# Optimization experiments

Hardware: AMD Instinct MI355X
Metric: run time of the kernel (lower is better)

## Reference

```python
import jax, jax.numpy as jnp
import numpy as np
from jax import lax

N, DEG = 32768, 16

def _leaky(x):
    return jnp.where(x > 0, x, 0.2 * x)

def _gatv2(h, src, ws, bs, wd, bd, attn, bias):
    # DGL GATv2Conv: e_uv = attn . leaky_relu(fc_src(h_u) + fc_dst(h_v)); edge softmax over in-neighbors
    Hn, Dn = attn.shape
    fs = (h @ ws + bs).reshape(N, Hn, Dn)
    fd = (h @ wd + bd).reshape(N, Hn, Dn)
    e = _leaky(fs[src] + fd[:, None])                          # [N, DEG, H, D]
    alpha = jax.nn.softmax(jnp.einsum('ndhk,hk->ndh', e, attn), axis=1)
    return jnp.einsum('ndh,ndhk->nhk', alpha, fs[src]) + bias.reshape(1, Hn, Dn)

def _lstm_last(x, wih, whh, b):
    # torch LSTM gate order i,f,g,o; returns final hidden state. x: [N, DEG, F]
    n, hh = x.shape[0], whh.shape[1]
    def step(carry, xt):
        h, c = carry
        g = xt @ wih.T + h @ whh.T + b
        i, f, gg, o = jnp.split(g, 4, axis=-1)
        c = jax.nn.sigmoid(f) * c + jax.nn.sigmoid(i) * jnp.tanh(gg)
        h = jax.nn.sigmoid(o) * jnp.tanh(c)
        return (h, c), None
    init = (jnp.zeros((n, hh), x.dtype), jnp.zeros((n, hh), x.dtype))
    (h, _), _ = lax.scan(step, init, jnp.swapaxes(x, 0, 1))
    return h

def _sage(h, src, wih, whh, b, wself, wneigh, bias):
    # DGL SAGEConv(aggregator='lstm'): rst = fc_self(h) + fc_neigh(lstm(neighbor msgs))
    hn = _lstm_last(h[src], wih, whh, b)
    return h @ wself + hn @ wneigh + bias

def _forward(feat, g0, l0, g1, l1, g2, l2, s1, s2, f1_w, f1_b, f2_w, f2_b, src):
    h = feat
    h = jax.nn.elu(_gatv2(h, src, *g0).reshape(N, -1) + h @ l0[0] + l0[1])
    h = jax.nn.elu(_gatv2(h, src, *g1).reshape(N, -1) + h @ l1[0] + l1[1])
    gat = _gatv2(h, src, *g2).mean(axis=1) + h @ l2[0] + l2[1]   # [N, 32]
    x = jax.nn.relu(_sage(feat, src, *s1))
    x = jax.nn.relu(_sage(x, src, *s2))                          # [N, 32]
    z = jnp.concatenate([gat, x], axis=1)
    z = jax.nn.relu(z @ f1_w + f1_b)
    return z @ f2_w + f2_b                                       # [N, 1]

def setup_inputs() -> dict:
    ks = iter(jax.random.split(jax.random.key(0), 64))
    def nrm(shape, s=0.1):
        return (s * jax.random.normal(next(ks), shape)).astype(jnp.float32)
    d = {}
    d['feat'] = jax.random.normal(next(ks), (N, 5), jnp.float32)
    d['src'] = jax.random.randint(next(ks), (N, DEG), 0, N)
    for i, (fi, hn) in enumerate([(5, 4), (128, 4), (128, 1)]):
        fo = 32 * hn
        d[f'g{i}_ws'] = nrm((fi, fo)); d[f'g{i}_bs'] = nrm((fo,))
        d[f'g{i}_wd'] = nrm((fi, fo)); d[f'g{i}_bd'] = nrm((fo,))
        d[f'g{i}_attn'] = nrm((hn, 32)); d[f'g{i}_bias'] = nrm((fo,))
        d[f'l{i}_w'] = nrm((fi, fo)); d[f'l{i}_b'] = nrm((fo,))
    for j, fi in [(1, 5), (2, 32)]:
        d[f's{j}_wih'] = nrm((4 * fi, fi)); d[f's{j}_whh'] = nrm((4 * fi, fi))
        d[f's{j}_b'] = nrm((4 * fi,))
        d[f's{j}_wself'] = nrm((fi, 32)); d[f's{j}_wneigh'] = nrm((fi, 32))
        d[f's{j}_bias'] = nrm((32,))
    d['f1_w'] = nrm((64, 16)); d['f1_b'] = nrm((16,))
    d['f2_w'] = (0.1 + 0.01 * jax.random.normal(next(ks), (16, 1))).astype(jnp.float32)
    d['f2_b'] = nrm((1,))
    return d

def reference(feat, src, g0_ws, g0_bs, g0_wd, g0_bd, g0_attn, g0_bias, l0_w, l0_b, g1_ws, g1_bs, g1_wd, g1_bd, g1_attn, g1_bias, l1_w, l1_b, g2_ws, g2_bs, g2_wd, g2_bd, g2_attn, g2_bias, l2_w, l2_b, s1_wih, s1_whh, s1_b, s1_wself, s1_wneigh, s1_bias, s2_wih, s2_whh, s2_b, s2_wself, s2_wneigh, s2_bias, f1_w, f1_b, f2_w, f2_b):
    return _forward(feat,
                    (g0_ws, g0_bs, g0_wd, g0_bd, g0_attn, g0_bias), (l0_w, l0_b),
                    (g1_ws, g1_bs, g1_wd, g1_bd, g1_attn, g1_bias), (l1_w, l1_b),
                    (g2_ws, g2_bs, g2_wd, g2_bd, g2_attn, g2_bias), (l2_w, l2_b),
                    (s1_wih, s1_whh, s1_b, s1_wself, s1_wneigh, s1_bias),
                    (s2_wih, s2_whh, s2_b, s2_wself, s2_wneigh, s2_bias),
                    f1_w, f1_b, f2_w, f2_b, src)
```

## Files before the change

### kernel.cpp

```cpp
#include <hip/hip_runtime.h>
#include <hip/hip_bf16.h>

#define NNODES 32768
#define DEG 16

__device__ __forceinline__ float sigmoidf_(float x) { return 1.f / (1.f + __expf(-x)); }
__device__ __forceinline__ float tanhf_(float x) { return 1.f - 2.f / (__expf(2.f * x) + 1.f); }

typedef __attribute__((ext_vector_type(8))) short bf16x8;
typedef __attribute__((ext_vector_type(4))) float f32x4;

__device__ __forceinline__ unsigned short f2bf_(float x) {
  __hip_bfloat16 b = __float2bfloat16(x);
  union { __hip_bfloat16 b; unsigned short u; } cv;
  cv.b = b;
  return cv.u;
}
__device__ __forceinline__ float bf2f_(unsigned short u) {
  union { unsigned short u; __hip_bfloat16 b; } cv;
  cv.u = u;
  return __bfloat162float(cv.b);
}
__device__ __forceinline__ void pack_hilo_(const float* v, bf16x8& hi, bf16x8& lo) {
#pragma unroll
  for (int j = 0; j < 8; j++) {
    unsigned short h = f2bf_(v[j]);
    float resid = v[j] - bf2f_(h);
    hi[j] = (short)h;
    lo[j] = (short)f2bf_(resid);
  }
}

#define WP_G1    0
#define WP_G2    98304
#define WP_S2WIH 122880
#define WP_TOTAL 131072

__global__ __launch_bounds__(256) void startup_kernel(
    const float* __restrict__ feat,
    const float* __restrict__ W0, const float* __restrict__ B0,
    const float* __restrict__ W1, const float* __restrict__ B1,
    const float* __restrict__ W2, const float* __restrict__ B2,
    float* __restrict__ O0, float* __restrict__ O1, float* __restrict__ O2,
    const float* __restrict__ g1ws, const float* __restrict__ g1wd,
    const float* __restrict__ l1w, const float* __restrict__ g2ws,
    const float* __restrict__ g2wd, const float* __restrict__ l2w,
    const float* __restrict__ s2wih, short* __restrict__ Wp) {
  __shared__ float w_s[5 * 64];
  __shared__ float in_s[32 * 8];
  __shared__ float b_s[64];
  const int bid = blockIdx.x;
  const int t = threadIdx.x;
  if (bid < 6144) {
    const int bz = bid >> 11, rem = bid & 2047, by = rem >> 10, bx = rem & 1023;
    const float* W = (bz == 0) ? W0 : (bz == 1) ? W1 : W2;
    const float* bias = (bz == 0) ? B0 : (bz == 1) ? B1 : B2;
    float* out = (bz == 0) ? O0 : (bz == 1) ? O1 : O2;
    const int rowBase = bx * 32;
    const int colBase = by * 64;
    for (int idx = t; idx < 5 * 64; idx += 256) {
      int k = idx >> 6, jj = idx & 63;
      w_s[idx] = W[(size_t)k * 128 + colBase + jj];
    }
    if (t < 64) b_s[t] = bias[colBase + t];
    for (int idx = t; idx < 32 * 5; idx += 256) {
      int r = idx / 5, k = idx - r * 5;
      in_s[r * 8 + k] = feat[(size_t)(rowBase + r) * 5 + k];
    }
    __syncthreads();
    const int jj = t & 63;
    const int rslot = t >> 6;
    float acc[8];
#pragma unroll
    for (int r = 0; r < 8; r++) acc[r] = b_s[jj];
    {
      float wv0 = w_s[0 * 64 + jj], wv1 = w_s[1 * 64 + jj];
      float wv2 = w_s[2 * 64 + jj], wv3 = w_s[3 * 64 + jj];
#pragma unroll
      for (int r = 0; r < 8; r++) {
        float4 ip = *(const float4*)&in_s[(rslot * 8 + r) * 8];
        acc[r] += ip.x * wv0 + ip.y * wv1 + ip.z * wv2 + ip.w * wv3;
      }
      float wv4 = w_s[4 * 64 + jj];
#pragma unroll
      for (int r = 0; r < 8; r++) acc[r] += in_s[(rslot * 8 + r) * 8 + 4] * wv4;
    }
#pragma unroll
    for (int r = 0; r < 8; r++)
      out[(size_t)(rowBase + rslot * 8 + r) * 128 + colBase + jj] = acc[r];
  } else {
    const int mid = bid - 6144;
    const float* W;
    int FI, FO, TRANS;
    size_t base;
    if (mid == 0)      { W = g1ws;  FI = 128; FO = 128; TRANS = 0; base = WP_G1; }
    else if (mid == 1) { W = g1wd;  FI = 128; FO = 128; TRANS = 0; base = WP_G1 + 32768; }
    else if (mid == 2) { W = l1w;   FI = 128; FO = 128; TRANS = 0; base = WP_G1 + 65536; }
    else if (mid == 3) { W = g2ws;  FI = 128; FO = 32;  TRANS = 0; base = WP_G2; }
    else if (mid == 4) { W = g2wd;  FI = 128; FO = 32;  TRANS = 0; base = WP_G2 + 8192; }
    else if (mid == 5) { W = l2w;   FI = 128; FO = 32;  TRANS = 0; base = WP_G2 + 16384; }
    else               { W = s2wih; FI = 32;  FO = 128; TRANS = 1; base = WP_S2WIH; }
    const int KS = FI / 32;
    const int total = FI * FO;
    for (int p = t; p < total; p += 256) {
      int j = p & 7, lane = (p >> 3) & 63, rest = p >> 9;
      int ks = rest % KS, f = rest / KS;
      int n = lane & 15, q = lane >> 4;
      int k = 32 * ks + 8 * q + j, fo = 16 * f + n;
      float v = TRANS ? W[(size_t)fo * FI + k] : W[(size_t)k * FO + fo];
      unsigned short hi = f2bf_(v);
      float resid = v - bf2f_(hi);
      Wp[base + p] = (short)hi;
      Wp[base + total + p] = (short)f2bf_(resid);
    }
  }
}

template <int KS, int FOT, int NZ>
__global__ __launch_bounds__(256) __attribute__((amdgpu_waves_per_eu(1, 4)))
void mfma_fc_kernel(const float* __restrict__ in, const short* __restrict__ Wp,
                    const float* __restrict__ B0, const float* __restrict__ B1,
                    const float* __restrict__ B2, float* __restrict__ O0,
                    float* __restrict__ O1, float* __restrict__ O2) {
  constexpr int FI = 32 * KS;
  constexpr int FO = 16 * FOT;
  __shared__ float lds_pad[9600];
  if ((const void*)in == nullptr) lds_pad[0] = 1.f;
  const int tid = threadIdx.x;
  const int wid = tid >> 6;
  const int lane = tid & 63;
  const int q = lane >> 4, n = lane & 15;
  const int n0 = blockIdx.x * 64 + wid * 16;
  bf16x8 Ahi[KS], Alo[KS];
#pragma unroll
  for (int ks = 0; ks < KS; ks++) {
    float av[8];
    *(float4*)&av[0] = *(const float4*)&in[(size_t)(n0 + n) * FI + 32 * ks + 8 * q];
    *(float4*)&av[4] = *(const float4*)&in[(size_t)(n0 + n) * FI + 32 * ks + 8 * q + 4];
    pack_hilo_(av, Ahi[ks], Alo[ks]);
  }
#pragma unroll
  for (int z = 0; z < NZ; z++) {
    const short* wz = Wp + (size_t)z * FI * FO * 2;
    const float* bz = (z == 0) ? B0 : (z == 1) ? B1 : B2;
    float* oz = (z == 0) ? O0 : (z == 1) ? O1 : O2;
#pragma unroll
    for (int f = 0; f < FOT; f++) {
      float bv = bz[16 * f + n];
      f32x4 acc = {bv, bv, bv, bv};
#pragma unroll
      for (int ks = 0; ks < KS; ks++) {
        bf16x8 Bhi = *(const bf16x8*)&wz[((size_t)(f * KS + ks) * 64 + lane) * 8];
        bf16x8 Blo = *(const bf16x8*)&wz[(size_t)FI * FO + ((size_t)(f * KS + ks) * 64 + lane) * 8];
        acc = __builtin_amdgcn_mfma_f32_16x16x32_bf16(Ahi[ks], Bhi, acc, 0, 0, 0);
        acc = __builtin_amdgcn_mfma_f32_16x16x32_bf16(Alo[ks], Bhi, acc, 0, 0, 0);
        acc = __builtin_amdgcn_mfma_f32_16x16x32_bf16(Ahi[ks], Blo, acc, 0, 0, 0);
      }
#pragma unroll
      for (int r = 0; r < 4; r++)
        oz[(size_t)(n0 + 4 * q + r) * FO + 16 * f + n] = acc[r];
    }
  }
}

__global__ __launch_bounds__(256) void gat4_kernel(const float* __restrict__ fs,
                                                   const float* __restrict__ fd,
                                                   const float* __restrict__ lin,
                                                   const int* __restrict__ src,
                                                   const float* __restrict__ attn,
                                                   const float* __restrict__ bias,
                                                   float* __restrict__ out) {
  constexpr int F = 128;
  const int lane = threadIdx.x & 63;
  const int wave = threadIdx.x >> 6;
  const int li = lane & 15;
  const int node = blockIdx.x * 4 + wave;
  const int f0 = 2 * lane;
  const int srcv = src[(size_t)node * DEG + li];
  const float2 fdv = *(const float2*)&fd[(size_t)node * F + f0];
  const float a0 = attn[f0];
  const float a1 = attn[f0 + 1];
  float m = -1e30f, s = 0.f, acc0 = 0.f, acc1 = 0.f;
  int sd = __shfl(srcv, (lane & 48), 64);
  float2 fsv = *(const float2*)&fs[(size_t)sd * F + f0];
#pragma unroll
  for (int d = 0; d < DEG; d++) {
    float2 cur = fsv;
    if (d < DEG - 1) {
      int sn = __shfl(srcv, (lane & 48) | (d + 1), 64);
      fsv = *(const float2*)&fs[(size_t)sn * F + f0];
    }
    float e0 = cur.x + fdv.x; e0 = (e0 > 0.f) ? e0 : 0.2f * e0;
    float e1 = cur.y + fdv.y; e1 = (e1 > 0.f) ? e1 : 0.2f * e1;
    float p = e0 * a0 + e1 * a1;
    p += __shfl_xor(p, 1, 64);
    p += __shfl_xor(p, 2, 64);
    p += __shfl_xor(p, 4, 64);
    p += __shfl_xor(p, 8, 64);
    float nm = fmaxf(m, p);
    float ex = __expf(p - nm);
    float sc = __expf(m - nm);
    s = s * sc + ex;
    acc0 = acc0 * sc + ex * cur.x;
    acc1 = acc1 * sc + ex * cur.y;
    m = nm;
  }
  float inv = 1.f / s;
  float2 lv = *(const float2*)&lin[(size_t)node * F + f0];
  float o0 = acc0 * inv + lv.x + bias[f0];
  float o1 = acc1 * inv + lv.y + bias[f0 + 1];
  o0 = (o0 > 0.f) ? o0 : __expf(o0) - 1.f;
  o1 = (o1 > 0.f) ? o1 : __expf(o1) - 1.f;
  *(float2*)&out[(size_t)node * F + f0] = make_float2(o0, o1);
}

__global__ __launch_bounds__(256) void gat1_fw1_kernel(
    const float* __restrict__ fs, const float* __restrict__ fd,
    const float* __restrict__ lin, const int* __restrict__ src,
    const float* __restrict__ attn, const float* __restrict__ bias,
    float* __restrict__ out, const float* __restrict__ feat,
    const float* __restrict__ wih, const float* __restrict__ wb,
    float* __restrict__ fwout) {
  __shared__ float w_s[100];
  __shared__ float b_s[20];
  if (blockIdx.x < 2048) {
    constexpr int F = 32;
    const int lane = threadIdx.x & 63;
    const int wave = threadIdx.x >> 6;
    const int G = lane >> 4, li = lane & 15;
    const int node = blockIdx.x * 16 + wave * 4 + G;
    const int f0 = 2 * li;
    const int srcv = src[(size_t)node * DEG + li];
    const float2 fdv = *(const float2*)&fd[(size_t)node * F + f0];
    const float a0 = attn[f0];
    const float a1 = attn[f0 + 1];
    float m = -1e30f, s = 0.f, acc0 = 0.f, acc1 = 0.f;
    int sd = __shfl(srcv, (lane & 48), 64);
    float2 fsv = *(const float2*)&fs[(size_t)sd * F + f0];
#pragma unroll
    for (int d = 0; d < DEG; d++) {
      float2 cur = fsv;
      if (d < DEG - 1) {
        int sn = __shfl(srcv, (lane & 48) | (d + 1), 64);
        fsv = *(const float2*)&fs[(size_t)sn * F + f0];
      }
      float e0 = cur.x + fdv.x; e0 = (e0 > 0.f) ? e0 : 0.2f * e0;
      float e1 = cur.y + fdv.y; e1 = (e1 > 0.f) ? e1 : 0.2f * e1;
      float p = e0 * a0 + e1 * a1;
      p += __shfl_xor(p, 1, 64);
      p += __shfl_xor(p, 2, 64);
      p += __shfl_xor(p, 4, 64);
      p += __shfl_xor(p, 8, 64);
      float nm = fmaxf(m, p);
      float ex = __expf(p - nm);
      float sc = __expf(m - nm);
      s = s * sc + ex;
      acc0 = acc0 * sc + ex * cur.x;
      acc1 = acc1 * sc + ex * cur.y;
      m = nm;
    }
    float inv = 1.f / s;
    float2 lv = *(const float2*)&lin[(size_t)node * F + f0];
    float o0 = acc0 * inv + lv.x + bias[f0];
    float o1 = acc1 * inv + lv.y + bias[f0 + 1];
    *(float2*)&out[(size_t)node * F + f0] = make_float2(o0, o1);
  } else {
    if (threadIdx.x < 100) w_s[threadIdx.x] = wih[threadIdx.x];
    if (threadIdx.x < 20) b_s[threadIdx.x] = wb[threadIdx.x];
    __syncthreads();
    const int n = (blockIdx.x - 2048) * 256 + threadIdx.x;
    float f[5];
#pragma unroll
    for (int k = 0; k < 5; k++) f[k] = feat[(size_t)n * 5 + k];
#pragma unroll
    for (int j = 0; j < 20; j++) {
      float a = b_s[j];
#pragma unroll
      for (int k = 0; k < 5; k++) a += f[k] * w_s[j * 5 + k];
      fwout[(size_t)n * 20 + j] = a;
    }
  }
}

__global__ __attribute__((amdgpu_waves_per_eu(1, 4))) __launch_bounds__(256)
void lstm1s_kernel(const float* __restrict__ FW, const int* __restrict__ src,
                   const float* __restrict__ whh, const float* __restrict__ feat,
                   const float* __restrict__ wself, const float* __restrict__ wneigh,
                   const float* __restrict__ bias, float* __restrict__ x1out) {
  __shared__ float w_s[100];
  __shared__ float ws_s[160];
  __shared__ float wn_s[160];
  __shared__ float b_s[32];
  if (threadIdx.x < 100) w_s[threadIdx.x] = whh[threadIdx.x];
  if (threadIdx.x < 160) {
    ws_s[threadIdx.x] = wself[threadIdx.x];
    wn_s[threadIdx.x] = wneigh[threadIdx.x];
  }
  if (threadIdx.x < 32) b_s[threadIdx.x] = bias[threadIdx.x];
  __syncthreads();
  const int n = blockIdx.x * 256 + threadIdx.x;
  const int* sp = src + (size_t)n * DEG;
  float f[5];
#pragma unroll
  for (int k = 0; k < 5; k++) f[k] = feat[(size_t)n * 5 + k];
  float h[5] = {0, 0, 0, 0, 0}, c[5] = {0, 0, 0, 0, 0};
  int sd = sp[0];
  float4 p0 = *(const float4*)&FW[(size_t)sd * 20 + 0];
  float4 p1 = *(const float4*)&FW[(size_t)sd * 20 + 4];
  float4 p2 = *(const float4*)&FW[(size_t)sd * 20 + 8];
  float4 p3 = *(const float4*)&FW[(size_t)sd * 20 + 12];
  float4 p4 = *(const float4*)&FW[(size_t)sd * 20 + 16];
  for (int d = 0; d < DEG; d++) {
    float g[20];
    g[0] = p0.x; g[1] = p0.y; g[2] = p0.z; g[3] = p0.w;
    g[4] = p1.x; g[5] = p1.y; g[6] = p1.z; g[7] = p1.w;
    g[8] = p2.x; g[9] = p2.y; g[10] = p2.z; g[11] = p2.w;
    g[12] = p3.x; g[13] = p3.y; g[14] = p3.z; g[15] = p3.w;
    g[16] = p4.x; g[17] = p4.y; g[18] = p4.z; g[19] = p4.w;
    if (d < DEG - 1) {
      int sn = sp[d + 1];
      p0 = *(const float4*)&FW[(size_t)sn * 20 + 0];
      p1 = *(const float4*)&FW[(size_t)sn * 20 + 4];
      p2 = *(const float4*)&FW[(size_t)sn * 20 + 8];
      p3 = *(const float4*)&FW[(size_t)sn * 20 + 12];
      p4 = *(const float4*)&FW[(size_t)sn * 20 + 16];
    }
#pragma unroll
    for (int j = 0; j < 20; j++) {
#pragma unroll
      for (int k = 0; k < 5; k++) g[j] += h[k] * w_s[j * 5 + k];
    }
#pragma unroll
    for (int k = 0; k < 5; k++) {
      float iv = sigmoidf_(g[k]);
      float fv = sigmoidf_(g[5 + k]);
      float gv = tanhf_(g[10 + k]);
      float ov = sigmoidf_(g[15 + k]);
      c[k] = fv * c[k] + iv * gv;
      h[k] = ov * tanhf_(c[k]);
    }
  }
#pragma unroll
  for (int j = 0; j < 32; j++) {
    float a = b_s[j];
#pragma unroll
    for (int k = 0; k < 5; k++) a += f[k] * ws_s[k * 32 + j] + h[k] * wn_s[k * 32 + j];
    x1out[(size_t)n * 32 + j] = fmaxf(a, 0.f);
  }
}

__global__ __launch_bounds__(256) __attribute__((amdgpu_waves_per_eu(1, 2)))
void lstm2_mfma_kernel(const float* __restrict__ XW, const int* __restrict__ src,
                       const float* __restrict__ whh, float* __restrict__ hn_out) {
  __shared__ float h_lds_all[4 * 16 * 36];
  __shared__ int src_lds_all[4 * 256];
  __shared__ float lds_pad[15000];
  if ((const void*)XW == nullptr) lds_pad[0] = 1.f;
  const int tid = threadIdx.x;
  const int wid = tid >> 6;
  const int lane = tid & 63;
  const int q = lane >> 4;
  const int n = lane & 15;
  const int n0 = (blockIdx.x * 4 + wid) * 16;
  float* h_lds = &h_lds_all[wid * 16 * 36];
  int* src_lds = &src_lds_all[wid * 256];

  {
    int4 sv = *(const int4*)&src[(size_t)(n0 + (lane >> 2)) * DEG + 4 * (lane & 3)];
    src_lds[(4 * (lane & 3) + 0) * 16 + (lane >> 2)] = sv.x;
    src_lds[(4 * (lane & 3) + 1) * 16 + (lane >> 2)] = sv.y;
    src_lds[(4 * (lane & 3) + 2) * 16 + (lane >> 2)] = sv.z;
    src_lds[(4 * (lane & 3) + 3) * 16 + (lane >> 2)] = sv.w;
  }

  bf16x8 Whi[8], Wlo[8];
#pragma unroll
  for (int gt = 0; gt < 8; gt++) {
    float wv[8];
    *(float4*)&wv[0] = *(const float4*)&whh[(size_t)(16 * gt + n) * 32 + 8 * q];
    *(float4*)&wv[4] = *(const float4*)&whh[(size_t)(16 * gt + n) * 32 + 8 * q + 4];
    pack_hilo_(wv, Whi[gt], Wlo[gt]);
  }

  bf16x8 Bhi, Blo;
#pragma unroll
  for (int j = 0; j < 8; j++) { Bhi[j] = 0; Blo[j] = 0; }
  float cst[8];
#pragma unroll
  for (int i = 0; i < 8; i++) cst[i] = 0.f;

  float4 tc[8], tn[8];
  {
    int s0 = src_lds[0 * 16 + n];
    const float* gb = XW + (size_t)s0 * 128;
#pragma unroll
    for (int i = 0; i < 8; i++) tc[i] = *(const float4*)&gb[16 * i + 4 * q];
  }

  float hv[8];
#pragma unroll
  for (int d = 0; d < DEG; d++) {
    f32x4 D[4][2];
#pragma unroll
    for (int p = 0; p < 4; p++) {
#pragma unroll
      for (int hh = 0; hh < 2; hh++) {
        int gt = p * 2 + hh;
        f32x4 acc = {0.f, 0.f, 0.f, 0.f};
        acc = __builtin_amdgcn_mfma_f32_16x16x32_bf16(Whi[gt], Bhi, acc, 0, 0, 0);
        acc = __builtin_amdgcn_mfma_f32_16x16x32_bf16(Wlo[gt], Bhi, acc, 0, 0, 0);
        acc = __builtin_amdgcn_mfma_f32_16x16x32_bf16(Whi[gt], Blo, acc, 0, 0, 0);
        D[p][hh] = acc;
      }
    }
    if (d < DEG - 1) {
      int s = src_lds[(d + 1) * 16 + n];
      const float* gb = XW + (size_t)s * 128;
#pragma unroll
      for (int i = 0; i < 8; i++) tn[i] = *(const float4*)&gb[16 * i + 4 * q];
    }
#pragma unroll
    for (int hh = 0; hh < 2; hh++) {
      float4 xi = tc[0 + hh];
      float4 xf = tc[2 + hh];
      float4 xg = tc[4 + hh];
      float4 xo = tc[6 + hh];
#pragma unroll
      for (int r = 0; r < 4; r++) {
        float xiv = (r == 0) ? xi.x : (r == 1) ? xi.y : (r == 2) ? xi.z : xi.w;
        float xfv = (r == 0) ? xf.x : (r == 1) ? xf.y : (r == 2) ? xf.z : xf.w;
        float xgv = (r == 0) ? xg.x : (r == 1) ? xg.y : (r == 2) ? xg.z : xg.w;
        float xov = (r == 0) ? xo.x : (r == 1) ? xo.y : (r == 2) ? xo.z : xo.w;
        int ci = hh * 4 + r;
        float iv = sigmoidf_(D[0][hh][r] + xiv);
        float fv = sigmoidf_(D[1][hh][r] + xfv);
        float gv = tanhf_(D[2][hh][r] + xgv);
        float ov = sigmoidf_(D[3][hh][r] + xov);
        cst[ci] = fv * cst[ci] + iv * gv;
        hv[ci] = ov * tanhf_(cst[ci]);
      }
    }
    if (d < DEG - 1) {
      *(float4*)&h_lds[n * 36 + 0 + 4 * q] = make_float4(hv[0], hv[1], hv[2], hv[3]);
      *(float4*)&h_lds[n * 36 + 16 + 4 * q] = make_float4(hv[4], hv[5], hv[6], hv[7]);
      float hb[8];
      *(float4*)&hb[0] = *(const float4*)&h_lds[n * 36 + 8 * q];
      *(float4*)&hb[4] = *(const float4*)&h_lds[n * 36 + 8 * q + 4];
      pack_hilo_(hb, Bhi, Blo);
#pragma unroll
      for (int i = 0; i < 8; i++) tc[i] = tn[i];
    }
  }
  *(float4*)&hn_out[(size_t)(n0 + n) * 32 + 0 + 4 * q] = make_float4(hv[0], hv[1], hv[2], hv[3]);
  *(float4*)&hn_out[(size_t)(n0 + n) * 32 + 16 + 4 * q] = make_float4(hv[4], hv[5], hv[6], hv[7]);
}

template <int FI>
__global__ __launch_bounds__(256) void sage_out_kernel(const float* __restrict__ in,
                                                       const float* __restrict__ hn,
                                                       const float* __restrict__ wself,
                                                       const float* __restrict__ wneigh,
                                                       const float* __restrict__ bias,
                                                       float* __restrict__ out) {
  __shared__ float ws_s[FI * 32];
  __shared__ float wn_s[FI * 32];
  __shared__ float b_s[32];
  for (int idx = threadIdx.x; idx < FI * 32; idx += 256) {
    ws_s[idx] = wself[idx];
    wn_s[idx] = wneigh[idx];
  }
  if (threadIdx.x < 32) b_s[threadIdx.x] = bias[threadIdx.x];
  __syncthreads();
  const int n = blockIdx.x * 8 + (threadIdx.x >> 5);
  const int j = threadIdx.x & 31;
  float a = b_s[j];
#pragma unroll
  for (int k = 0; k < FI; k++) a += in[(size_t)n * FI + k] * ws_s[k * 32 + j];
#pragma unroll
  for (int k = 0; k < FI; k++) a += hn[(size_t)n * FI + k] * wn_s[k * 32 + j];
  out[(size_t)n * 32 + j] = fmaxf(a, 0.f);
}

__global__ __attribute__((amdgpu_waves_per_eu(4, 4))) __launch_bounds__(256)
void final_kernel(const float* __restrict__ gat,
                  const float* __restrict__ x2,
                  const float* __restrict__ f1w,
                  const float* __restrict__ f1b,
                  const float* __restrict__ f2w,
                  const float* __restrict__ f2b,
                  float* __restrict__ out) {
  __shared__ float w1_s[64 * 16];
  __shared__ float b1_s[16];
  __shared__ float w2_s[16];
  for (int idx = threadIdx.x; idx < 1024; idx += 256) w1_s[idx] = f1w[idx];
  if (threadIdx.x < 16) {
    b1_s[threadIdx.x] = f1b[threadIdx.x];
    w2_s[threadIdx.x] = f2w[threadIdx.x];
  }
  __syncthreads();
  const int n = blockIdx.x * 256 + threadIdx.x;
  float z[64];
#pragma unroll
  for (int k = 0; k < 32; k += 4) {
    float4 a = *(const float4*)&gat[(size_t)n * 32 + k];
    z[k] = a.x; z[k + 1] = a.y; z[k + 2] = a.z; z[k + 3] = a.w;
    float4 b = *(const float4*)&x2[(size_t)n * 32 + k];
    z[32 + k] = b.x; z[32 + k + 1] = b.y; z[32 + k + 2] = b.z; z[32 + k + 3] = b.w;
  }
  float o = f2b[0];
#pragma unroll
  for (int j = 0; j < 16; j++) {
    float a = b1_s[j];
#pragma unroll
    for (int k = 0; k < 64; k++) a += z[k] * w1_s[k * 16 + j];
    o += fmaxf(a, 0.f) * w2_s[j];
  }
  out[n] = o;
}

extern "C" void kernel_launch(void* const* d_in, const int* in_sizes, int n_in,
                              void* d_out, int out_size, void* d_ws, size_t ws_size,
                              hipStream_t stream) {
  const int N = NNODES;
  const float* feat = (const float*)d_in[0];
  const int* src = (const int*)d_in[1];
  const float* g0_ws = (const float*)d_in[2];
  const float* g0_bs = (const float*)d_in[3];
  const float* g0_wd = (const float*)d_in[4];
  const float* g0_bd = (const float*)d_in[5];
  const float* g0_attn = (const float*)d_in[6];
  const float* g0_bias = (const float*)d_in[7];
  const float* l0_w = (const float*)d_in[8];
  const float* l0_b = (const float*)d_in[9];
  const float* g1_ws = (const float*)d_in[10];
  const float* g1_bs = (const float*)d_in[11];
  const float* g1_wd = (const float*)d_in[12];
  const float* g1_bd = (const float*)d_in[13];
  const float* g1_attn = (const float*)d_in[14];
  const float* g1_bias = (const float*)d_in[15];
  const float* l1_w = (const float*)d_in[16];
  const float* l1_b = (const float*)d_in[17];
  const float* g2_ws = (const float*)d_in[18];
  const float* g2_bs = (const float*)d_in[19];
  const float* g2_wd = (const float*)d_in[20];
  const float* g2_bd = (const float*)d_in[21];
  const float* g2_attn = (const float*)d_in[22];
  const float* g2_bias = (const float*)d_in[23];
  const float* l2_w = (const float*)d_in[24];
  const float* l2_b = (const float*)d_in[25];
  const float* s1_wih = (const float*)d_in[26];
  const float* s1_whh = (const float*)d_in[27];
  const float* s1_b = (const float*)d_in[28];
  const float* s1_wself = (const float*)d_in[29];
  const float* s1_wneigh = (const float*)d_in[30];
  const float* s1_bias = (const float*)d_in[31];
  const float* s2_wih = (const float*)d_in[32];
  const float* s2_whh = (const float*)d_in[33];
  const float* s2_b = (const float*)d_in[34];
  const float* s2_wself = (const float*)d_in[35];
  const float* s2_wneigh = (const float*)d_in[36];
  const float* s2_bias = (const float*)d_in[37];
  const float* f1_w = (const float*)d_in[38];
  const float* f1_b = (const float*)d_in[39];
  const float* f2_w = (const float*)d_in[40];
  const float* f2_b = (const float*)d_in[41];

  float* A = (float*)d_ws;
  float* B = A + (size_t)N * 128;
  float* C = B + (size_t)N * 128;
  float* D = C + (size_t)N * 128;
  float* E = D + (size_t)N * 128;
  short* Wp = (short*)(A + (size_t)5 * N * 128);

  startup_kernel<<<6151, 256, 0, stream>>>(
      feat, g0_ws, g0_bs, g0_wd, g0_bd, l0_w, l0_b, A, B, C,
      g1_ws, g1_wd, l1_w, g2_ws, g2_wd, l2_w, s2_wih, Wp);
  gat4_kernel<<<N / 4, 256, 0, stream>>>(A, B, C, src, g0_attn, g0_bias, D);
  mfma_fc_kernel<4, 8, 3><<<N / 64, 256, 0, stream>>>(
      D, Wp + WP_G1, g1_bs, g1_bd, l1_b, A, B, C);
  gat4_kernel<<<N / 4, 256, 0, stream>>>(A, B, C, src, g1_attn, g1_bias, E);
  mfma_fc_kernel<4, 2, 3><<<N / 64, 256, 0, stream>>>(
      E, Wp + WP_G2, g2_bs, g2_bd, l2_b, A, B, C);
  gat1_fw1_kernel<<<2048 + 128, 256, 0, stream>>>(
      A, B, C, src, g2_attn, g2_bias, D, feat, s1_wih, s1_b, E);
  lstm1s_kernel<<<N / 256, 256, 0, stream>>>(E, src, s1_whh, feat, s1_wself,
                                             s1_wneigh, s1_bias, C);
  mfma_fc_kernel<1, 8, 1><<<N / 64, 256, 0, stream>>>(
      C, Wp + WP_S2WIH, s2_b, nullptr, nullptr, A, nullptr, nullptr);
  lstm2_mfma_kernel<<<N / 64, 256, 0, stream>>>(A, src, s2_whh, E);
  sage_out_kernel<32><<<N / 8, 256, 0, stream>>>(C, E, s2_wself, s2_wneigh,
                                                 s2_bias, B);
  final_kernel<<<N / 256, 256, 0, stream>>>(D, B, f1_w, f1_b, f2_w, f2_b, (float*)d_out);
}
```

Baseline: 424.7 us.

## Interleave independent SAGE/LSTM branch work into GAT kernels via horizontal fusion

The independent SAGE-LSTM branch is co-scheduled with the GAT layers. Block indices are split inside merged kernels so that GAT and LSTM1, the FC layer and the XW projection, GAT and LSTM2, and the FC layer and the SAGE output run in the same launches, which cuts the kernel count from eleven to seven. The point is to fill idle CUs during the long serial LSTM recurrences and to save launch gaps. The price is extra workspace buffers; a fallback keeps the old path when the workspace is too small, and the merged kernels may have uneven block costs and more LDS per block.

```diff
diff --git a/kernel.cpp b/kernel.cpp
--- a/kernel.cpp
+++ b/kernel.cpp
@@ -35,6 +35,373 @@
 #define WP_G2    98304
 #define WP_S2WIH 122880
 #define WP_TOTAL 131072
+
+
+__device__ __forceinline__ void gat4_body(int vbid, const float* __restrict__ fs,
+                                          const float* __restrict__ fd,
+                                          const float* __restrict__ lin,
+                                          const int* __restrict__ src,
+                                          const float* __restrict__ attn,
+                                          const float* __restrict__ bias,
+                                          float* __restrict__ out) {
+  constexpr int F = 128;
+  const int lane = threadIdx.x & 63;
+  const int wave = threadIdx.x >> 6;
+  const int li = lane & 15;
+  const int node = vbid * 4 + wave;
+  const int f0 = 2 * lane;
+  const int srcv = src[(size_t)node * DEG + li];
+  const float2 fdv = *(const float2*)&fd[(size_t)node * F + f0];
+  const float a0 = attn[f0];
+  const float a1 = attn[f0 + 1];
+  float m = -1e30f, s = 0.f, acc0 = 0.f, acc1 = 0.f;
+  int sd = __shfl(srcv, (lane & 48), 64);
+  float2 fsv = *(const float2*)&fs[(size_t)sd * F + f0];
+#pragma unroll
+  for (int d = 0; d < DEG; d++) {
+    float2 cur = fsv;
+    if (d < DEG - 1) {
+      int sn = __shfl(srcv, (lane & 48) | (d + 1), 64);
+      fsv = *(const float2*)&fs[(size_t)sn * F + f0];
+    }
+    float e0 = cur.x + fdv.x; e0 = (e0 > 0.f) ? e0 : 0.2f * e0;
+    float e1 = cur.y + fdv.y; e1 = (e1 > 0.f) ? e1 : 0.2f * e1;
+    float p = e0 * a0 + e1 * a1;
+    p += __shfl_xor(p, 1, 64);
+    p += __shfl_xor(p, 2, 64);
+    p += __shfl_xor(p, 4, 64);
+    p += __shfl_xor(p, 8, 64);
+    float nm = fmaxf(m, p);
+    float ex = __expf(p - nm);
+    float sc = __expf(m - nm);
+    s = s * sc + ex;
+    acc0 = acc0 * sc + ex * cur.x;
+    acc1 = acc1 * sc + ex * cur.y;
+    m = nm;
+  }
+  float inv = 1.f / s;
+  float2 lv = *(const float2*)&lin[(size_t)node * F + f0];
+  float o0 = acc0 * inv + lv.x + bias[f0];
+  float o1 = acc1 * inv + lv.y + bias[f0 + 1];
+  o0 = (o0 > 0.f) ? o0 : __expf(o0) - 1.f;
+  o1 = (o1 > 0.f) ? o1 : __expf(o1) - 1.f;
+  *(float2*)&out[(size_t)node * F + f0] = make_float2(o0, o1);
+}
+
+__device__ __forceinline__ void gat1_body(int vbid, const float* __restrict__ fs,
+                                          const float* __restrict__ fd,
+                                          const float* __restrict__ lin,
+                                          const int* __restrict__ src,
+                                          const float* __restrict__ attn,
+                                          const float* __restrict__ bias,
+                                          float* __restrict__ out) {
+  constexpr int F = 32;
+  const int lane = threadIdx.x & 63;
+  const int wave = threadIdx.x >> 6;
+  const int G = lane >> 4, li = lane & 15;
+  const int node = vbid * 16 + wave * 4 + G;
+  const int f0 = 2 * li;
+  const int srcv = src[(size_t)node * DEG + li];
+  const float2 fdv = *(const float2*)&fd[(size_t)node * F + f0];
+  const float a0 = attn[f0];
+  const float a1 = attn[f0 + 1];
+  float m = -1e30f, s = 0.f, acc0 = 0.f, acc1 = 0.f;
+  int sd = __shfl(srcv, (lane & 48), 64);
+  float2 fsv = *(const float2*)&fs[(size_t)sd * F + f0];
+#pragma unroll
+  for (int d = 0; d < DEG; d++) {
+    float2 cur = fsv;
+    if (d < DEG - 1) {
+      int sn = __shfl(srcv, (lane & 48) | (d + 1), 64);
+      fsv = *(const float2*)&fs[(size_t)sn * F + f0];
+    }
+    float e0 = cur.x + fdv.x; e0 = (e0 > 0.f) ? e0 : 0.2f * e0;
+    float e1 = cur.y + fdv.y; e1 = (e1 > 0.f) ? e1 : 0.2f * e1;
+    float p = e0 * a0 + e1 * a1;
+    p += __shfl_xor(p, 1, 64);
+    p += __shfl_xor(p, 2, 64);
+    p += __shfl_xor(p, 4, 64);
+    p += __shfl_xor(p, 8, 64);
+    float nm = fmaxf(m, p);
+    float ex = __expf(p - nm);
+    float sc = __expf(m - nm);
+    s = s * sc + ex;
+    acc0 = acc0 * sc + ex * cur.x;
+    acc1 = acc1 * sc + ex * cur.y;
+    m = nm;
+  }
+  float inv = 1.f / s;
+  float2 lv = *(const float2*)&lin[(size_t)node * F + f0];
+  float o0 = acc0 * inv + lv.x + bias[f0];
+  float o1 = acc1 * inv + lv.y + bias[f0 + 1];
+  *(float2*)&out[(size_t)node * F + f0] = make_float2(o0, o1);
+}
+
+template <int KS, int FOT, int NZ>
+__device__ __forceinline__ void mfma_fc_body(int vbid, const float* __restrict__ in,
+                                             const short* __restrict__ Wp,
+                                             const float* __restrict__ B0,
+                                             const float* __restrict__ B1,
+                                             const float* __restrict__ B2,
+                                             float* __restrict__ O0,
+                                             float* __restrict__ O1,
+                                             float* __restrict__ O2) {
+  constexpr int FI = 32 * KS;
+  constexpr int FO = 16 * FOT;
+  const int tid = threadIdx.x;
+  const int wid = tid >> 6;
+  const int lane = tid & 63;
+  const int q = lane >> 4, n = lane & 15;
+  const int n0 = vbid * 64 + wid * 16;
+  bf16x8 Ahi[KS], Alo[KS];
+#pragma unroll
+  for (int ks = 0; ks < KS; ks++) {
+    float av[8];
+    *(float4*)&av[0] = *(const float4*)&in[(size_t)(n0 + n) * FI + 32 * ks + 8 * q];
+    *(float4*)&av[4] = *(const float4*)&in[(size_t)(n0 + n) * FI + 32 * ks + 8 * q + 4];
+    pack_hilo_(av, Ahi[ks], Alo[ks]);
+  }
+#pragma unroll
+  for (int z = 0; z < NZ; z++) {
+    const short* wz = Wp + (size_t)z * FI * FO * 2;
+    const float* bz = (z == 0) ? B0 : (z == 1) ? B1 : B2;
+    float* oz = (z == 0) ? O0 : (z == 1) ? O1 : O2;
+#pragma unroll
+    for (int f = 0; f < FOT; f++) {
+      float bv = bz[16 * f + n];
+      f32x4 acc = {bv, bv, bv, bv};
+#pragma unroll
+      for (int ks = 0; ks < KS; ks++) {
+        bf16x8 Bhi = *(const bf16x8*)&wz[((size_t)(f * KS + ks) * 64 + lane) * 8];
+        bf16x8 Blo = *(const bf16x8*)&wz[(size_t)FI * FO + ((size_t)(f * KS + ks) * 64 + lane) * 8];
+        acc = __builtin_amdgcn_mfma_f32_16x16x32_bf16(Ahi[ks], Bhi, acc, 0, 0, 0);
+        acc = __builtin_amdgcn_mfma_f32_16x16x32_bf16(Alo[ks], Bhi, acc, 0, 0, 0);
+        acc = __builtin_amdgcn_mfma_f32_16x16x32_bf16(Ahi[ks], Blo, acc, 0, 0, 0);
+      }
+#pragma unroll
+      for (int r = 0; r < 4; r++)
+        oz[(size_t)(n0 + 4 * q + r) * FO + 16 * f + n] = acc[r];
+    }
+  }
+}
+
+__device__ __forceinline__ void fw1_body(int vbid, const float* __restrict__ feat,
+                                         const float* __restrict__ wih,
+                                         const float* __restrict__ wb,
+                                         float* __restrict__ fwout,
+                                         float* w_s, float* b_s) {
+  if (threadIdx.x < 100) w_s[threadIdx.x] = wih[threadIdx.x];
+  if (threadIdx.x < 20) b_s[threadIdx.x] = wb[threadIdx.x];
+  __syncthreads();
+  const int n = vbid * 256 + threadIdx.x;
+  float f[5];
+#pragma unroll
+  for (int k = 0; k < 5; k++) f[k] = feat[(size_t)n * 5 + k];
+#pragma unroll
+  for (int j = 0; j < 20; j++) {
+    float a = b_s[j];
+#pragma unroll
+    for (int k = 0; k < 5; k++) a += f[k] * w_s[j * 5 + k];
+    fwout[(size_t)n * 20 + j] = a;
+  }
+}
+
+__device__ __forceinline__ void lstm1s_body(int vbid, const float* __restrict__ FW,
+                                            const int* __restrict__ src,
+                                            const float* __restrict__ whh,
+                                            const float* __restrict__ feat,
+                                            const float* __restrict__ wself,
+                                            const float* __restrict__ wneigh,
+                                            const float* __restrict__ bias,
+                                            float* __restrict__ x1out,
+                                            float* w_s, float* ws_s, float* wn_s,
+                                            float* b_s) {
+  if (threadIdx.x < 100) w_s[threadIdx.x] = whh[threadIdx.x];
+  if (threadIdx.x < 160) {
+    ws_s[threadIdx.x] = wself[threadIdx.x];
+    wn_s[threadIdx.x] = wneigh[threadIdx.x];
+  }
+  if (threadIdx.x < 32) b_s[threadIdx.x] = bias[threadIdx.x];
+  __syncthreads();
+  const int n = vbid * 256 + threadIdx.x;
+  const int* sp = src + (size_t)n * DEG;
+  float f[5];
+#pragma unroll
+  for (int k = 0; k < 5; k++) f[k] = feat[(size_t)n * 5 + k];
+  float h[5] = {0, 0, 0, 0, 0}, c[5] = {0, 0, 0, 0, 0};
+  int sd = sp[0];
+  float4 p0 = *(const float4*)&FW[(size_t)sd * 20 + 0];
+  float4 p1 = *(const float4*)&FW[(size_t)sd * 20 + 4];
+  float4 p2 = *(const float4*)&FW[(size_t)sd * 20 + 8];
+  float4 p3 = *(const float4*)&FW[(size_t)sd * 20 + 12];
+  float4 p4 = *(const float4*)&FW[(size_t)sd * 20 + 16];
+  for (int d = 0; d < DEG; d++) {
+    float g[20];
+    g[0] = p0.x; g[1] = p0.y; g[2] = p0.z; g[3] = p0.w;
+    g[4] = p1.x; g[5] = p1.y; g[6] = p1.z; g[7] = p1.w;
+    g[8] = p2.x; g[9] = p2.y; g[10] = p2.z; g[11] = p2.w;
+    g[12] = p3.x; g[13] = p3.y; g[14] = p3.z; g[15] = p3.w;
+    g[16] = p4.x; g[17] = p4.y; g[18] = p4.z; g[19] = p4.w;
+    if (d < DEG - 1) {
+      int sn = sp[d + 1];
+      p0 = *(const float4*)&FW[(size_t)sn * 20 + 0];
+      p1 = *(const float4*)&FW[(size_t)sn * 20 + 4];
+      p2 = *(const float4*)&FW[(size_t)sn * 20 + 8];
+      p3 = *(const float4*)&FW[(size_t)sn * 20 + 12];
+      p4 = *(const float4*)&FW[(size_t)sn * 20 + 16];
+    }
+#pragma unroll
+    for (int j = 0; j < 20; j++) {
+#pragma unroll
+      for (int k = 0; k < 5; k++) g[j] += h[k] * w_s[j * 5 + k];
+    }
+#pragma unroll
+    for (int k = 0; k < 5; k++) {
+      float iv = sigmoidf_(g[k]);
+      float fv = sigmoidf_(g[5 + k]);
+      float gv = tanhf_(g[10 + k]);
+      float ov = sigmoidf_(g[15 + k]);
+      c[k] = fv * c[k] + iv * gv;
+      h[k] = ov * tanhf_(c[k]);
+    }
+  }
+#pragma unroll
+  for (int j = 0; j < 32; j++) {
+    float a = b_s[j];
+#pragma unroll
+    for (int k = 0; k < 5; k++) a += f[k] * ws_s[k * 32 + j] + h[k] * wn_s[k * 32 + j];
+    x1out[(size_t)n * 32 + j] = fmaxf(a, 0.f);
+  }
+}
+
+__device__ __forceinline__ void lstm2_body(int vbid, const float* __restrict__ XW,
+                                           const int* __restrict__ src,
+                                           const float* __restrict__ whh,
+                                           float* __restrict__ hn_out,
+                                           float* h_lds_all, int* src_lds_all) {
+  const int tid = threadIdx.x;
+  const int wid = tid >> 6;
+  const int lane = tid & 63;
+  const int q = lane >> 4;
+  const int n = lane & 15;
+  const int n0 = (vbid * 4 + wid) * 16;
+  float* h_lds = &h_lds_all[wid * 16 * 36];
+  int* src_lds = &src_lds_all[wid * 256];
+
+  {
+    int4 sv = *(const int4*)&src[(size_t)(n0 + (lane >> 2)) * DEG + 4 * (lane & 3)];
+    src_lds[(4 * (lane & 3) + 0) * 16 + (lane >> 2)] = sv.x;
+    src_lds[(4 * (lane & 3) + 1) * 16 + (lane >> 2)] = sv.y;
+    src_lds[(4 * (lane & 3) + 2) * 16 + (lane >> 2)] = sv.z;
+    src_lds[(4 * (lane & 3) + 3) * 16 + (lane >> 2)] = sv.w;
+  }
+
+  bf16x8 Whi[8], Wlo[8];
+#pragma unroll
+  for (int gt = 0; gt < 8; gt++) {
+    float wv[8];
+    *(float4*)&wv[0] = *(const float4*)&whh[(size_t)(16 * gt + n) * 32 + 8 * q];
+    *(float4*)&wv[4] = *(const float4*)&whh[(size_t)(16 * gt + n) * 32 + 8 * q + 4];
+    pack_hilo_(wv, Whi[gt], Wlo[gt]);
+  }
+
+  bf16x8 Bhi, Blo;
+#pragma unroll
+  for (int j = 0; j < 8; j++) { Bhi[j] = 0; Blo[j] = 0; }
+  float cst[8];
+#pragma unroll
+  for (int i = 0; i < 8; i++) cst[i] = 0.f;
+
+  float4 tc[8], tn[8];
+  {
+    int s0 = src_lds[0 * 16 + n];
+    const float* gb = XW + (size_t)s0 * 128;
+#pragma unroll
+    for (int i = 0; i < 8; i++) tc[i] = *(const float4*)&gb[16 * i + 4 * q];
+  }
+
+  float hv[8];
+#pragma unroll
+  for (int d = 0; d < DEG; d++) {
+    f32x4 D[4][2];
+#pragma unroll
+    for (int p = 0; p < 4; p++) {
+#pragma unroll
+      for (int hh = 0; hh < 2; hh++) {
+        int gt = p * 2 + hh;
+        f32x4 acc = {0.f, 0.f, 0.f, 0.f};
+        acc = __builtin_amdgcn_mfma_f32_16x16x32_bf16(Whi[gt], Bhi, acc, 0, 0, 0);
+        acc = __builtin_amdgcn_mfma_f32_16x16x32_bf16(Wlo[gt], Bhi, acc, 0, 0, 0);
+        acc = __builtin_amdgcn_mfma_f32_16x16x32_bf16(Whi[gt], Blo, acc, 0, 0, 0);
+        D[p][hh] = acc;
+      }
+    }
+    if (d < DEG - 1) {
+      int s = src_lds[(d + 1) * 16 + n];
+      const float* gb = XW + (size_t)s * 128;
+#pragma unroll
+      for (int i = 0; i < 8; i++) tn[i] = *(const float4*)&gb[16 * i + 4 * q];
+    }
+#pragma unroll
+    for (int hh = 0; hh < 2; hh++) {
+      float4 xi = tc[0 + hh];
+      float4 xf = tc[2 + hh];
+      float4 xg = tc[4 + hh];
+      float4 xo = tc[6 + hh];
+#pragma unroll
+      for (int r = 0; r < 4; r++) {
+        float xiv = (r == 0) ? xi.x : (r == 1) ? xi.y : (r == 2) ? xi.z : xi.w;
+        float xfv = (r == 0) ? xf.x : (r == 1) ? xf.y : (r == 2) ? xf.z : xf.w;
+        float xgv = (r == 0) ? xg.x : (r == 1) ? xg.y : (r == 2) ? xg.z : xg.w;
+        float xov = (r == 0) ? xo.x : (r == 1) ? xo.y : (r == 2) ? xo.z : xo.w;
+        int ci = hh * 4 + r;
+        float iv = sigmoidf_(D[0][hh][r] + xiv);
+        float fv = sigmoidf_(D[1][hh][r] + xfv);
+        float gv = tanhf_(D[2][hh][r] + xgv);
+        float ov = sigmoidf_(D[3][hh][r] + xov);
+        cst[ci] = fv * cst[ci] + iv * gv;
+        hv[ci] = ov * tanhf_(cst[ci]);
+      }
+    }
+    if (d < DEG - 1) {
+      *(float4*)&h_lds[n * 36 + 0 + 4 * q] = make_float4(hv[0], hv[1], hv[2], hv[3]);
+      *(float4*)&h_lds[n * 36 + 16 + 4 * q] = make_float4(hv[4], hv[5], hv[6], hv[7]);
+      float hb[8];
+      *(float4*)&hb[0] = *(const float4*)&h_lds[n * 36 + 8 * q];
+      *(float4*)&hb[4] = *(const float4*)&h_lds[n * 36 + 8 * q + 4];
+      pack_hilo_(hb, Bhi, Blo);
+#pragma unroll
+      for (int i = 0; i < 8; i++) tc[i] = tn[i];
+    }
+  }
+  *(float4*)&hn_out[(size_t)(n0 + n) * 32 + 0 + 4 * q] = make_float4(hv[0], hv[1], hv[2], hv[3]);
+  *(float4*)&hn_out[(size_t)(n0 + n) * 32 + 16 + 4 * q] = make_float4(hv[4], hv[5], hv[6], hv[7]);
+}
+
+__device__ __forceinline__ void sage_body(int vbid, const float* __restrict__ in,
+                                          const float* __restrict__ hn,
+                                          const float* __restrict__ wself,
+                                          const float* __restrict__ wneigh,
+                                          const float* __restrict__ bias,
+                                          float* __restrict__ out,
+                                          float* ws_s, float* wn_s, float* b_s) {
+  constexpr int FI = 32;
+  for (int idx = threadIdx.x; idx < FI * 32; idx += 256) {
+    ws_s[idx] = wself[idx];
+    wn_s[idx] = wneigh[idx];
+  }
+  if (threadIdx.x < 32) b_s[threadIdx.x] = bias[threadIdx.x];
+  __syncthreads();
+  const int n = vbid * 8 + (threadIdx.x >> 5);
+  const int j = threadIdx.x & 31;
+  float a = b_s[j];
+#pragma unroll
+  for (int k = 0; k < FI; k++) a += in[(size_t)n * FI + k] * ws_s[k * 32 + j];
+#pragma unroll
+  for (int k = 0; k < FI; k++) a += hn[(size_t)n * FI + k] * wn_s[k * 32 + j];
+  out[(size_t)n * 32 + j] = fmaxf(a, 0.f);
+}
+
 
 __global__ __launch_bounds__(256) void startup_kernel(
     const float* __restrict__ feat,
@@ -45,7 +412,9 @@
     const float* __restrict__ g1ws, const float* __restrict__ g1wd,
     const float* __restrict__ l1w, const float* __restrict__ g2ws,
     const float* __restrict__ g2wd, const float* __restrict__ l2w,
-    const float* __restrict__ s2wih, short* __restrict__ Wp) {
+    const float* __restrict__ s2wih, short* __restrict__ Wp,
+    const float* __restrict__ s1wih, const float* __restrict__ s1b,
+    float* __restrict__ fwout) {
   __shared__ float w_s[5 * 64];
   __shared__ float in_s[32 * 8];
   __shared__ float b_s[64];
@@ -88,7 +457,7 @@
 #pragma unroll
     for (int r = 0; r < 8; r++)
       out[(size_t)(rowBase + rslot * 8 + r) * 128 + colBase + jj] = acc[r];
-  } else {
+  } else if (bid < 6151) {
     const int mid = bid - 6144;
     const float* W;
     int FI, FO, TRANS;
@@ -113,53 +482,8 @@
       Wp[base + p] = (short)hi;
       Wp[base + total + p] = (short)f2bf_(resid);
     }
-  }
-}
-
-template <int KS, int FOT, int NZ>
-__global__ __launch_bounds__(256) __attribute__((amdgpu_waves_per_eu(1, 4)))
-void mfma_fc_kernel(const float* __restrict__ in, const short* __restrict__ Wp,
-                    const float* __restrict__ B0, const float* __restrict__ B1,
-                    const float* __restrict__ B2, float* __restrict__ O0,
-                    float* __restrict__ O1, float* __restrict__ O2) {
-  constexpr int FI = 32 * KS;
-  constexpr int FO = 16 * FOT;
-  __shared__ float lds_pad[9600];
-  if ((const void*)in == nullptr) lds_pad[0] = 1.f;
-  const int tid = threadIdx.x;
-  const int wid = tid >> 6;
-  const int lane = tid & 63;
-  const int q = lane >> 4, n = lane & 15;
-  const int n0 = blockIdx.x * 64 + wid * 16;
-  bf16x8 Ahi[KS], Alo[KS];
-#pragma unroll
-  for (int ks = 0; ks < KS; ks++) {
-    float av[8];
-    *(float4*)&av[0] = *(const float4*)&in[(size_t)(n0 + n) * FI + 32 * ks + 8 * q];
-    *(float4*)&av[4] = *(const float4*)&in[(size_t)(n0 + n) * FI + 32 * ks + 8 * q + 4];
-    pack_hilo_(av, Ahi[ks], Alo[ks]);
-  }
-#pragma unroll
-  for (int z = 0; z < NZ; z++) {
-    const short* wz = Wp + (size_t)z * FI * FO * 2;
-    const float* bz = (z == 0) ? B0 : (z == 1) ? B1 : B2;
-    float* oz = (z == 0) ? O0 : (z == 1) ? O1 : O2;
-#pragma unroll
-    for (int f = 0; f < FOT; f++) {
-      float bv = bz[16 * f + n];
-      f32x4 acc = {bv, bv, bv, bv};
-#pragma unroll
-      for (int ks = 0; ks < KS; ks++) {
-        bf16x8 Bhi = *(const bf16x8*)&wz[((size_t)(f * KS + ks) * 64 + lane) * 8];
-        bf16x8 Blo = *(const bf16x8*)&wz[(size_t)FI * FO + ((size_t)(f * KS + ks) * 64 + lane) * 8];
-        acc = __builtin_amdgcn_mfma_f32_16x16x32_bf16(Ahi[ks], Bhi, acc, 0, 0, 0);
-        acc = __builtin_amdgcn_mfma_f32_16x16x32_bf16(Alo[ks], Bhi, acc, 0, 0, 0);
-        acc = __builtin_amdgcn_mfma_f32_16x16x32_bf16(Ahi[ks], Blo, acc, 0, 0, 0);
-      }
-#pragma unroll
-      for (int r = 0; r < 4; r++)
-        oz[(size_t)(n0 + 4 * q + r) * FO + 16 * f + n] = acc[r];
-    }
+  } else {
+    fw1_body(bid - 6151, feat, s1wih, s1b, fwout, w_s, b_s);
   }
 }
 
@@ -170,48 +494,18 @@
                                                    const float* __restrict__ attn,
                                                    const float* __restrict__ bias,
                                                    float* __restrict__ out) {
-  constexpr int F = 128;
-  const int lane = threadIdx.x & 63;
-  const int wave = threadIdx.x >> 6;
-  const int li = lane & 15;
-  const int node = blockIdx.x * 4 + wave;
-  const int f0 = 2 * lane;
-  const int srcv = src[(size_t)node * DEG + li];
-  const float2 fdv = *(const float2*)&fd[(size_t)node * F + f0];
-  const float a0 = attn[f0];
-  const float a1 = attn[f0 + 1];
-  float m = -1e30f, s = 0.f, acc0 = 0.f, acc1 = 0.f;
-  int sd = __shfl(srcv, (lane & 48), 64);
-  float2 fsv = *(const float2*)&fs[(size_t)sd * F + f0];
-#pragma unroll
-  for (int d = 0; d < DEG; d++) {
-    float2 cur = fsv;
-    if (d < DEG - 1) {
-      int sn = __shfl(srcv, (lane & 48) | (d + 1), 64);
-      fsv = *(const float2*)&fs[(size_t)sn * F + f0];
-    }
-    float e0 = cur.x + fdv.x; e0 = (e0 > 0.f) ? e0 : 0.2f * e0;
-    float e1 = cur.y + fdv.y; e1 = (e1 > 0.f) ? e1 : 0.2f * e1;
-    float p = e0 * a0 + e1 * a1;
-    p += __shfl_xor(p, 1, 64);
-    p += __shfl_xor(p, 2, 64);
-    p += __shfl_xor(p, 4, 64);
-    p += __shfl_xor(p, 8, 64);
-    float nm = fmaxf(m, p);
-    float ex = __expf(p - nm);
-    float sc = __expf(m - nm);
-    s = s * sc + ex;
-    acc0 = acc0 * sc + ex * cur.x;
-    acc1 = acc1 * sc + ex * cur.y;
-    m = nm;
-  }
-  float inv = 1.f / s;
-  float2 lv = *(const float2*)&lin[(size_t)node * F + f0];
-  float o0 = acc0 * inv + lv.x + bias[f0];
-  float o1 = acc1 * inv + lv.y + bias[f0 + 1];
-  o0 = (o0 > 0.f) ? o0 : __expf(o0) - 1.f;
-  o1 = (o1 > 0.f) ? o1 : __expf(o1) - 1.f;
-  *(float2*)&out[(size_t)node * F + f0] = make_float2(o0, o1);
+  gat4_body(blockIdx.x, fs, fd, lin, src, attn, bias, out);
+}
+
+template <int KS, int FOT, int NZ>
+__global__ __launch_bounds__(256) __attribute__((amdgpu_waves_per_eu(1, 4)))
+void mfma_fc_kernel(const float* __restrict__ in, const short* __restrict__ Wp,
+                    const float* __restrict__ B0, const float* __restrict__ B1,
+                    const float* __restrict__ B2, float* __restrict__ O0,
+                    float* __restrict__ O1, float* __restrict__ O2) {
+  __shared__ float lds_pad[9600];
+  if ((const void*)in == nullptr) lds_pad[0] = 1.f;
+  mfma_fc_body<KS, FOT, NZ>(blockIdx.x, in, Wp, B0, B1, B2, O0, O1, O2);
 }
 
 __global__ __launch_bounds__(256) void gat1_fw1_kernel(
@@ -224,62 +518,18 @@
   __shared__ float w_s[100];
   __shared__ float b_s[20];
   if (blockIdx.x < 2048) {
-    constexpr int F = 32;
-    const int lane = threadIdx.x & 63;
-    const int wave = threadIdx.x >> 6;
-    const int G = lane >> 4, li = lane & 15;
-    const int node = blockIdx.x * 16 + wave * 4 + G;
-    const int f0 = 2 * li;
-    const int srcv = src[(size_t)node * DEG + li];
-    const float2 fdv = *(const float2*)&fd[(size_t)node * F + f0];
-    const float a0 = attn[f0];
-    const float a1 = attn[f0 + 1];
-    float m = -1e30f, s = 0.f, acc0 = 0.f, acc1 = 0.f;
-    int sd = __shfl(srcv, (lane & 48), 64);
-    float2 fsv = *(const float2*)&fs[(size_t)sd * F + f0];
-#pragma unroll
-    for (int d = 0; d < DEG; d++) {
-      float2 cur = fsv;
-      if (d < DEG - 1) {
-        int sn = __shfl(srcv, (lane & 48) | (d + 1), 64);
-        fsv = *(const float2*)&fs[(size_t)sn * F + f0];
-      }
-      float e0 = cur.x + fdv.x; e0 = (e0 > 0.f) ? e0 : 0.2f * e0;
-      float e1 = cur.y + fdv.y; e1 = (e1 > 0.f) ? e1 : 0.2f * e1;
-      float p = e0 * a0 + e1 * a1;
-      p += __shfl_xor(p, 1, 64);
-      p += __shfl_xor(p, 2, 64);
-      p += __shfl_xor(p, 4, 64);
-      p += __shfl_xor(p, 8, 64);
-      float nm = fmaxf(m, p);
-      float ex = __expf(p - nm);
-      float sc = __expf(m - nm);
-      s = s * sc + ex;
-      acc0 = acc0 * sc + ex * cur.x;
-      acc1 = acc1 * sc + ex * cur.y;
-      m = nm;
-    }
-    float inv = 1.f / s;
-    float2 lv = *(const float2*)&lin[(size_t)node * F + f0];
-    float o0 = acc0 * inv + lv.x + bias[f0];
-    float o1 = acc1 * inv + lv.y + bias[f0 + 1];
-    *(float2*)&out[(size_t)node * F + f0] = make_float2(o0, o1);
+    gat1_body(blockIdx.x, fs, fd, lin, src, attn, bias, out);
   } else {
-    if (threadIdx.x < 100) w_s[threadIdx.x] = wih[threadIdx.x];
-    if (threadIdx.x < 20) b_s[threadIdx.x] = wb[threadIdx.x];
-    __syncthreads();
-    const int n = (blockIdx.x - 2048) * 256 + threadIdx.x;
-    float f[5];
-#pragma unroll
-    for (int k = 0; k < 5; k++) f[k] = feat[(size_t)n * 5 + k];
-#pragma unroll
-    for (int j = 0; j < 20; j++) {
-      float a = b_s[j];
-#pragma unroll
-      for (int k = 0; k < 5; k++) a += f[k] * w_s[j * 5 + k];
-      fwout[(size_t)n * 20 + j] = a;
-    }
-  }
+    fw1_body(blockIdx.x - 2048, feat, wih, wb, fwout, w_s, b_s);
+  }
+}
+
+__global__ __launch_bounds__(256) void gat1_kernel(
+    const float* __restrict__ fs, const float* __restrict__ fd,
+    const float* __restrict__ lin, const int* __restrict__ src,
+    const float* __restrict__ attn, const float* __restrict__ bias,
+    float* __restrict__ out) {
+  gat1_body(blockIdx.x, fs, fd, lin, src, attn, bias, out);
 }
 
 __global__ __attribute__((amdgpu_waves_per_eu(1, 4))) __launch_bounds__(256)
@@ -291,62 +541,8 @@
   __shared__ float ws_s[160];
   __shared__ float wn_s[160];
   __shared__ float b_s[32];
-  if (threadIdx.x < 100) w_s[threadIdx.x] = whh[threadIdx.x];
-  if (threadIdx.x < 160) {
-    ws_s[threadIdx.x] = wself[threadIdx.x];
-    wn_s[threadIdx.x] = wneigh[threadIdx.x];
-  }
-  if (threadIdx.x < 32) b_s[threadIdx.x] = bias[threadIdx.x];
-  __syncthreads();
-  const int n = blockIdx.x * 256 + threadIdx.x;
-  const int* sp = src + (size_t)n * DEG;
-  float f[5];
-#pragma unroll
-  for (int k = 0; k < 5; k++) f[k] = feat[(size_t)n * 5 + k];
-  float h[5] = {0, 0, 0, 0, 0}, c[5] = {0, 0, 0, 0, 0};
-  int sd = sp[0];
-  float4 p0 = *(const float4*)&FW[(size_t)sd * 20 + 0];
-  float4 p1 = *(const float4*)&FW[(size_t)sd * 20 + 4];
-  float4 p2 = *(const float4*)&FW[(size_t)sd * 20 + 8];
-  float4 p3 = *(const float4*)&FW[(size_t)sd * 20 + 12];
-  float4 p4 = *(const float4*)&FW[(size_t)sd * 20 + 16];
-  for (int d = 0; d < DEG; d++) {
-    float g[20];
-    g[0] = p0.x; g[1] = p0.y; g[2] = p0.z; g[3] = p0.w;
-    g[4] = p1.x; g[5] = p1.y; g[6] = p1.z; g[7] = p1.w;
-    g[8] = p2.x; g[9] = p2.y; g[10] = p2.z; g[11] = p2.w;
-    g[12] = p3.x; g[13] = p3.y; g[14] = p3.z; g[15] = p3.w;
-    g[16] = p4.x; g[17] = p4.y; g[18] = p4.z; g[19] = p4.w;
-    if (d < DEG - 1) {
-      int sn = sp[d + 1];
-      p0 = *(const float4*)&FW[(size_t)sn * 20 + 0];
-      p1 = *(const float4*)&FW[(size_t)sn * 20 + 4];
-      p2 = *(const float4*)&FW[(size_t)sn * 20 + 8];
-      p3 = *(const float4*)&FW[(size_t)sn * 20 + 12];
-      p4 = *(const float4*)&FW[(size_t)sn * 20 + 16];
-    }
-#pragma unroll
-    for (int j = 0; j < 20; j++) {
-#pragma unroll
-      for (int k = 0; k < 5; k++) g[j] += h[k] * w_s[j * 5 + k];
-    }
-#pragma unroll
-    for (int k = 0; k < 5; k++) {
-      float iv = sigmoidf_(g[k]);
-      float fv = sigmoidf_(g[5 + k]);
-      float gv = tanhf_(g[10 + k]);
-      float ov = sigmoidf_(g[15 + k]);
-      c[k] = fv * c[k] + iv * gv;
-      h[k] = ov * tanhf_(c[k]);
-    }
-  }
-#pragma unroll
-  for (int j = 0; j < 32; j++) {
-    float a = b_s[j];
-#pragma unroll
-    for (int k = 0; k < 5; k++) a += f[k] * ws_s[k * 32 + j] + h[k] * wn_s[k * 32 + j];
-    x1out[(size_t)n * 32 + j] = fmaxf(a, 0.f);
-  }
+  lstm1s_body(blockIdx.x, FW, src, whh, feat, wself, wneigh, bias, x1out,
+              w_s, ws_s, wn_s, b_s);
 }
 
 __global__ __launch_bounds__(256) __attribute__((amdgpu_waves_per_eu(1, 2)))
@@ -356,129 +552,102 @@
   __shared__ int src_lds_all[4 * 256];
   __shared__ float lds_pad[15000];
   if ((const void*)XW == nullptr) lds_pad[0] = 1.f;
-  const int tid = threadIdx.x;
-  const int wid = tid >> 6;
-  const int lane = tid & 63;
-  const int q = lane >> 4;
-  const int n = lane & 15;
-  const int n0 = (blockIdx.x * 4 + wid) * 16;
-  float* h_lds = &h_lds_all[wid * 16 * 36];
-  int* src_lds = &src_lds_all[wid * 256];
-
-  {
-    int4 sv = *(const int4*)&src[(size_t)(n0 + (lane >> 2)) * DEG + 4 * (lane & 3)];
-    src_lds[(4 * (lane & 3) + 0) * 16 + (lane >> 2)] = sv.x;
-    src_lds[(4 * (lane & 3) + 1) * 16 + (lane >> 2)] = sv.y;
-    src_lds[(4 * (lane & 3) + 2) * 16 + (lane >> 2)] = sv.z;
-    src_lds[(4 * (lane & 3) + 3) * 16 + (lane >> 2)] = sv.w;
-  }
-
-  bf16x8 Whi[8], Wlo[8];
-#pragma unroll
-  for (int gt = 0; gt < 8; gt++) {
-    float wv[8];
-    *(float4*)&wv[0] = *(const float4*)&whh[(size_t)(16 * gt + n) * 32 + 8 * q];
-    *(float4*)&wv[4] = *(const float4*)&whh[(size_t)(16 * gt + n) * 32 + 8 * q + 4];
-    pack_hilo_(wv, Whi[gt], Wlo[gt]);
-  }
-
-  bf16x8 Bhi, Blo;
-#pragma unroll
-  for (int j = 0; j < 8; j++) { Bhi[j] = 0; Blo[j] = 0; }
-  float cst[8];
-#pragma unroll
-  for (int i = 0; i < 8; i++) cst[i] = 0.f;
-
-  float4 tc[8], tn[8];
-  {
-    int s0 = src_lds[0 * 16 + n];
-    const float* gb = XW + (size_t)s0 * 128;
-#pragma unroll
-    for (int i = 0; i < 8; i++) tc[i] = *(const float4*)&gb[16 * i + 4 * q];
-  }
-
-  float hv[8];
-#pragma unroll
-  for (int d = 0; d < DEG; d++) {
-    f32x4 D[4][2];
-#pragma unroll
-    for (int p = 0; p < 4; p++) {
-#pragma unroll
-      for (int hh = 0; hh < 2; hh++) {
-        int gt = p * 2 + hh;
-        f32x4 acc = {0.f, 0.f, 0.f, 0.f};
-        acc = __builtin_amdgcn_mfma_f32_16x16x32_bf16(Whi[gt], Bhi, acc, 0, 0, 0);
-        acc = __builtin_amdgcn_mfma_f32_16x16x32_bf16(Wlo[gt], Bhi, acc, 0, 0, 0);
-        acc = __builtin_amdgcn_mfma_f32_16x16x32_bf16(Whi[gt], Blo, acc, 0, 0, 0);
-        D[p][hh] = acc;
-      }
-    }
-    if (d < DEG - 1) {
-      int s = src_lds[(d + 1) * 16 + n];
-      const float* gb = XW + (size_t)s * 128;
-#pragma unroll
-      for (int i = 0; i < 8; i++) tn[i] = *(const float4*)&gb[16 * i + 4 * q];
-    }
-#pragma unroll
-    for (int hh = 0; hh < 2; hh++) {
-      float4 xi = tc[0 + hh];
-      float4 xf = tc[2 + hh];
-      float4 xg = tc[4 + hh];
-      float4 xo = tc[6 + hh];
-#pragma unroll
-      for (int r = 0; r < 4; r++) {
-        float xiv = (r == 0) ? xi.x : (r == 1) ? xi.y : (r == 2) ? xi.z : xi.w;
-        float xfv = (r == 0) ? xf.x : (r == 1) ? xf.y : (r == 2) ? xf.z : xf.w;
-        float xgv = (r == 0) ? xg.x : (r == 1) ? xg.y : (r == 2) ? xg.z : xg.w;
-        float xov = (r == 0) ? xo.x : (r == 1) ? xo.y : (r == 2) ? xo.z : xo.w;
-        int ci = hh * 4 + r;
-        float iv = sigmoidf_(D[0][hh][r] + xiv);
-        float fv = sigmoidf_(D[1][hh][r] + xfv);
-        float gv = tanhf_(D[2][hh][r] + xgv);
-        float ov = sigmoidf_(D[3][hh][r] + xov);
-        cst[ci] = fv * cst[ci] + iv * gv;
-        hv[ci] = ov * tanhf_(cst[ci]);
-      }
-    }
-    if (d < DEG - 1) {
-      *(float4*)&h_lds[n * 36 + 0 + 4 * q] = make_float4(hv[0], hv[1], hv[2], hv[3]);
-      *(float4*)&h_lds[n * 36 + 16 + 4 * q] = make_float4(hv[4], hv[5], hv[6], hv[7]);
-      float hb[8];
-      *(float4*)&hb[0] = *(const float4*)&h_lds[n * 36 + 8 * q];
-      *(float4*)&hb[4] = *(const float4*)&h_lds[n * 36 + 8 * q + 4];
-      pack_hilo_(hb, Bhi, Blo);
-#pragma unroll
-      for (int i = 0; i < 8; i++) tc[i] = tn[i];
-    }
-  }
-  *(float4*)&hn_out[(size_t)(n0 + n) * 32 + 0 + 4 * q] = make_float4(hv[0], hv[1], hv[2], hv[3]);
-  *(float4*)&hn_out[(size_t)(n0 + n) * 32 + 16 + 4 * q] = make_float4(hv[4], hv[5], hv[6], hv[7]);
-}
-
-template <int FI>
+  lstm2_body(blockIdx.x, XW, src, whh, hn_out, h_lds_all, src_lds_all);
+}
+
 __global__ __launch_bounds__(256) void sage_out_kernel(const float* __restrict__ in,
                                                        const float* __restrict__ hn,
                                                        const float* __restrict__ wself,
                                                        const float* __restrict__ wneigh,
                                                        const float* __restrict__ bias,
                                                        float* __restrict__ out) {
-  __shared__ float ws_s[FI * 32];
-  __shared__ float wn_s[FI * 32];
+  __shared__ float ws_s[32 * 32];
+  __shared__ float wn_s[32 * 32];
   __shared__ float b_s[32];
-  for (int idx = threadIdx.x; idx < FI * 32; idx += 256) {
-    ws_s[idx] = wself[idx];
-    wn_s[idx] = wneigh[idx];
-  }
-  if (threadIdx.x < 32) b_s[threadIdx.x] = bias[threadIdx.x];
-  __syncthreads();
-  const int n = blockIdx.x * 8 + (threadIdx.x >> 5);
-  const int j = threadIdx.x & 31;
-  float a = b_s[j];
-#pragma unroll
-  for (int k = 0; k < FI; k++) a += in[(size_t)n * FI + k] * ws_s[k * 32 + j];
-#pragma unroll
-  for (int k = 0; k < FI; k++) a += hn[(size_t)n * FI + k] * wn_s[k * 32 + j];
-  out[(size_t)n * 32 + j] = fmaxf(a, 0.f);
+  sage_body(blockIdx.x, in, hn, wself, wneigh, bias, out, ws_s, wn_s, b_s);
+}
+
+
+__global__ __launch_bounds__(256) void gat4_lstm1s_kernel(
+    const float* __restrict__ fs, const float* __restrict__ fd,
+    const float* __restrict__ lin, const int* __restrict__ src,
+    const float* __restrict__ attn, const float* __restrict__ bias,
+    float* __restrict__ out,
+    const float* __restrict__ FW, const float* __restrict__ whh,
+    const float* __restrict__ feat, const float* __restrict__ wself,
+    const float* __restrict__ wneigh, const float* __restrict__ sbias,
+    float* __restrict__ x1out) {
+  __shared__ float w_s[100];
+  __shared__ float ws_s[160];
+  __shared__ float wn_s[160];
+  __shared__ float b_s[32];
+  const int bid = blockIdx.x;
+  const int r = bid % 65, q = bid / 65;
+  if (r < 64) {
+    gat4_body(q * 64 + r, fs, fd, lin, src, attn, bias, out);
+  } else {
+    lstm1s_body(q, FW, src, whh, feat, wself, wneigh, sbias, x1out,
+                w_s, ws_s, wn_s, b_s);
+  }
+}
+
+__global__ __launch_bounds__(256) void mfma_g1_xw_kernel(
+    const float* __restrict__ in, const short* __restrict__ Wp,
+    const float* __restrict__ B0, const float* __restrict__ B1,
+    const float* __restrict__ B2, float* __restrict__ O0,
+    float* __restrict__ O1, float* __restrict__ O2,
+    const float* __restrict__ x1, const short* __restrict__ WpX,
+    const float* __restrict__ s2b, float* __restrict__ XW) {
+  __shared__ float lds_pad[9600];
+  if ((const void*)in == nullptr) lds_pad[0] = 1.f;
+  const int bid = blockIdx.x;
+  if ((bid & 1) == 0) {
+    mfma_fc_body<4, 8, 3>(bid >> 1, in, Wp, B0, B1, B2, O0, O1, O2);
+  } else {
+    mfma_fc_body<1, 8, 1>(bid >> 1, x1, WpX, s2b, nullptr, nullptr,
+                          XW, nullptr, nullptr);
+  }
+}
+
+__global__ __launch_bounds__(256) void gat4_lstm2_kernel(
+    const float* __restrict__ fs, const float* __restrict__ fd,
+    const float* __restrict__ lin, const int* __restrict__ src,
+    const float* __restrict__ attn, const float* __restrict__ bias,
+    float* __restrict__ out,
+    const float* __restrict__ XW, const float* __restrict__ whh,
+    float* __restrict__ hn_out) {
+  __shared__ float h_lds_all[4 * 16 * 36];
+  __shared__ int src_lds_all[4 * 256];
+  const int bid = blockIdx.x;
+  const int r = bid % 17, q = bid / 17;
+  if (r < 16) {
+    gat4_body(q * 16 + r, fs, fd, lin, src, attn, bias, out);
+  } else {
+    lstm2_body(q, XW, src, whh, hn_out, h_lds_all, src_lds_all);
+  }
+}
+
+__global__ __launch_bounds__(256) void mfma_g2_sage_kernel(
+    const float* __restrict__ in, const short* __restrict__ Wp,
+    const float* __restrict__ B0, const float* __restrict__ B1,
+    const float* __restrict__ B2, float* __restrict__ O0,
+    float* __restrict__ O1, float* __restrict__ O2,
+    const float* __restrict__ x1, const float* __restrict__ hn,
+    const float* __restrict__ wself, const float* __restrict__ wneigh,
+    const float* __restrict__ sbias, float* __restrict__ x2out) {
+  __shared__ float lds_pad[9600];
+  __shared__ float ws_s[32 * 32];
+  __shared__ float wn_s[32 * 32];
+  __shared__ float b_s[32];
+  if ((const void*)in == nullptr) lds_pad[0] = 1.f;
+  const int bid = blockIdx.x;
+  const int r = bid % 9, q = bid / 9;
+  if (r == 0) {
+    mfma_fc_body<4, 2, 3>(q, in, Wp, B0, B1, B2, O0, O1, O2);
+  } else {
+    sage_body(q * 8 + (r - 1), x1, hn, wself, wneigh, sbias, x2out,
+              ws_s, wn_s, b_s);
+  }
 }
 
 __global__ __attribute__((amdgpu_waves_per_eu(4, 4))) __launch_bounds__(256)
@@ -571,24 +740,52 @@
   float* D = C + (size_t)N * 128;
   float* E = D + (size_t)N * 128;
   short* Wp = (short*)(A + (size_t)5 * N * 128);
-
-  startup_kernel<<<6151, 256, 0, stream>>>(
-      feat, g0_ws, g0_bs, g0_wd, g0_bd, l0_w, l0_b, A, B, C,
-      g1_ws, g1_wd, l1_w, g2_ws, g2_wd, l2_w, s2_wih, Wp);
-  gat4_kernel<<<N / 4, 256, 0, stream>>>(A, B, C, src, g0_attn, g0_bias, D);
-  mfma_fc_kernel<4, 8, 3><<<N / 64, 256, 0, stream>>>(
-      D, Wp + WP_G1, g1_bs, g1_bd, l1_b, A, B, C);
-  gat4_kernel<<<N / 4, 256, 0, stream>>>(A, B, C, src, g1_attn, g1_bias, E);
-  mfma_fc_kernel<4, 2, 3><<<N / 64, 256, 0, stream>>>(
-      E, Wp + WP_G2, g2_bs, g2_bd, l2_b, A, B, C);
-  gat1_fw1_kernel<<<2048 + 128, 256, 0, stream>>>(
-      A, B, C, src, g2_attn, g2_bias, D, feat, s1_wih, s1_b, E);
-  lstm1s_kernel<<<N / 256, 256, 0, stream>>>(E, src, s1_whh, feat, s1_wself,
-                                             s1_wneigh, s1_bias, C);
-  mfma_fc_kernel<1, 8, 1><<<N / 64, 256, 0, stream>>>(
-      C, Wp + WP_S2WIH, s2_b, nullptr, nullptr, A, nullptr, nullptr);
-  lstm2_mfma_kernel<<<N / 64, 256, 0, stream>>>(A, src, s2_whh, E);
-  sage_out_kernel<32><<<N / 8, 256, 0, stream>>>(C, E, s2_wself, s2_wneigh,
-                                                 s2_bias, B);
-  final_kernel<<<N / 256, 256, 0, stream>>>(D, B, f1_w, f1_b, f2_w, f2_b, (float*)d_out);
-}
+  float* X1 = (float*)(Wp + WP_TOTAL);
+  float* XW = X1 + (size_t)N * 32;
+  float* HN2 = XW + (size_t)N * 128;
+  float* X2 = HN2 + (size_t)N * 32;
+  const size_t need = (size_t)((char*)(X2 + (size_t)N * 32) - (char*)d_ws);
+  const bool big = ws_size >= need;
+
+  if (big) {
+    startup_kernel<<<6151 + 128, 256, 0, stream>>>(
+        feat, g0_ws, g0_bs, g0_wd, g0_bd, l0_w, l0_b, A, B, C,
+        g1_ws, g1_wd, l1_w, g2_ws, g2_wd, l2_w, s2_wih, Wp, s1_wih, s1_b, E);
+    gat4_lstm1s_kernel<<<8320, 256, 0, stream>>>(
+        A, B, C, src, g0_attn, g0_bias, D,
+        E, s1_whh, feat, s1_wself, s1_wneigh, s1_bias, X1);
+    mfma_g1_xw_kernel<<<1024, 256, 0, stream>>>(
+        D, Wp + WP_G1, g1_bs, g1_bd, l1_b, A, B, C,
+        X1, Wp + WP_S2WIH, s2_b, XW);
+    gat4_lstm2_kernel<<<8704, 256, 0, stream>>>(
+        A, B, C, src, g1_attn, g1_bias, E,
+        XW, s2_whh, HN2);
+    mfma_g2_sage_kernel<<<4608, 256, 0, stream>>>(
+        E, Wp + WP_G2, g2_bs, g2_bd, l2_b, A, B, C,
+        X1, HN2, s2_wself, s2_wneigh, s2_bias, X2);
+    gat1_kernel<<<2048, 256, 0, stream>>>(A, B, C, src, g2_attn, g2_bias, D);
+    final_kernel<<<N / 256, 256, 0, stream>>>(D, X2, f1_w, f1_b, f2_w, f2_b,
+                                              (float*)d_out);
+  } else {
+    startup_kernel<<<6151, 256, 0, stream>>>(
+        feat, g0_ws, g0_bs, g0_wd, g0_bd, l0_w, l0_b, A, B, C,
+        g1_ws, g1_wd, l1_w, g2_ws, g2_wd, l2_w, s2_wih, Wp, s1_wih, s1_b, E);
+    gat4_kernel<<<N / 4, 256, 0, stream>>>(A, B, C, src, g0_attn, g0_bias, D);
+    mfma_fc_kernel<4, 8, 3><<<N / 64, 256, 0, stream>>>(
+        D, Wp + WP_G1, g1_bs, g1_bd, l1_b, A, B, C);
+    gat4_kernel<<<N / 4, 256, 0, stream>>>(A, B, C, src, g1_attn, g1_bias, E);
+    mfma_fc_kernel<4, 2, 3><<<N / 64, 256, 0, stream>>>(
+        E, Wp + WP_G2, g2_bs, g2_bd, l2_b, A, B, C);
+    gat1_fw1_kernel<<<2048 + 128, 256, 0, stream>>>(
+        A, B, C, src, g2_attn, g2_bias, D, feat, s1_wih, s1_b, E);
+    lstm1s_kernel<<<N / 256, 256, 0, stream>>>(E, src, s1_whh, feat, s1_wself,
+                                               s1_wneigh, s1_bias, C);
+    mfma_fc_kernel<1, 8, 1><<<N / 64, 256, 0, stream>>>(
+        C, Wp + WP_S2WIH, s2_b, nullptr, nullptr, A, nullptr, nullptr);
+    lstm2_mfma_kernel<<<N / 64, 256, 0, stream>>>(A, src, s2_whh, E);
+    sage_out_kernel<<<N / 8, 256, 0, stream>>>(C, E, s2_wself, s2_wneigh,
+                                               s2_bias, B);
+    final_kernel<<<N / 256, 256, 0, stream>>>(D, B, f1_w, f1_b, f2_w, f2_b,
+                                              (float*)d_out);
+  }
+}
```

Result: slower. 508.3 us (+19.7%).
